# Kernel tuning notes

Measured on AMD Instinct MI355X. Metric: run time of the kernel, lower is better.

The kernel has to match this reference:

```python
import jax, jax.numpy as jnp
import numpy as np

NUM_REGIONS = 29
OUT = 7          # RoIAlign output size
SR = 2           # sampling_ratio
IMG = 1024.0     # input image H = W
LN_EPS = 1e-5


def _layernorm(x, g, b):
    mu = jnp.mean(x, axis=-1, keepdims=True)
    var = jnp.mean(jnp.square(x - mu), axis=-1, keepdims=True)
    return (x - mu) * jax.lax.rsqrt(var + LN_EPS) * g + b


def _roi_align(fm, rois):
    """torchvision roi_align (aligned=False), spatial_scale=1.0, sampling_ratio=SR.
    fm: [B,C,H,W], rois: [B,R,4] (x1,y1,x2,y2 in feature coords). -> [B,R,C,OUT,OUT]"""
    B, C, H, W = fm.shape
    x1, y1, x2, y2 = jnp.moveaxis(rois, -1, 0)            # each [B,R]
    roi_w = jnp.maximum(x2 - x1, 1.0)
    roi_h = jnp.maximum(y2 - y1, 1.0)
    bw = roi_w / OUT
    bh = roi_h / OUT
    # sub-bin offsets: (bin + (s+0.5)/SR) for bin in [0,OUT), s in [0,SR)
    off = jnp.arange(OUT, dtype=jnp.float32)[:, None] + (jnp.arange(SR, dtype=jnp.float32)[None, :] + 0.5) / SR  # [OUT,SR]
    py = y1[..., None, None] + off * bh[..., None, None]  # [B,R,OUT,SR]
    px = x1[..., None, None] + off * bw[..., None, None]  # [B,R,OUT,SR]
    y = py[:, :, :, :, None, None]                        # [B,R,OUT,SR,1,1]
    x = px[:, :, None, None, :, :]                        # [B,R,1,1,OUT,SR]
    valid = (y >= -1.0) & (y <= H) & (x >= -1.0) & (x <= W)
    yc = jnp.clip(y, 0.0, H - 1.0)
    xc = jnp.clip(x, 0.0, W - 1.0)
    y0 = jnp.floor(yc).astype(jnp.int32)
    x0 = jnp.floor(xc).astype(jnp.int32)
    y1i = jnp.minimum(y0 + 1, H - 1)
    x1i = jnp.minimum(x0 + 1, W - 1)
    ly = yc - y0
    lx = xc - x0
    hy = 1.0 - ly
    hx = 1.0 - lx
    gather = jax.vmap(lambda f, yy, xx: f[:, yy, xx])     # per image: [C,H,W] -> [C,...]
    v00 = gather(fm, y0, x0)                              # [B,C,R,OUT,SR,OUT,SR]
    v01 = gather(fm, y0, x1i)
    v10 = gather(fm, y1i, x0)
    v11 = gather(fm, y1i, x1i)
    w00 = (hy * hx)[:, None]
    w01 = (hy * lx)[:, None]
    w10 = (ly * hx)[:, None]
    w11 = (ly * lx)[:, None]
    val = w00 * v00 + w01 * v01 + w10 * v10 + w11 * v11
    val = jnp.where(valid[:, None], val, 0.0)
    pooled = val.mean(axis=(4, 6))                        # average over SRxSR samples -> [B,C,R,OUT,OUT]
    return jnp.transpose(pooled, (0, 2, 1, 3, 4))         # [B,R,C,OUT,OUT]


def setup_inputs() -> dict:
    key = jax.random.key(0)
    ks = jax.random.split(key, 8)
    B, N, C, Hf, Wf, FD = 32, 40, 256, 64, 64, 768
    D = C * OUT * OUT
    feature_maps = jax.random.normal(ks[0], (B, C, Hf, Wf), jnp.float32)
    xy = jax.random.uniform(ks[1], (B, N, 2), jnp.float32) * 900.0
    wh = jax.random.uniform(ks[2], (B, N, 2), jnp.float32) * 100.0 + 16.0
    boxes = jnp.concatenate([xy, xy + wh], axis=-1)       # valid x1,y1,x2,y2 in image coords
    scores = jax.random.uniform(ks[3], (B, N), jnp.float32)
    labels = jax.random.randint(ks[4], (B, N), 0, NUM_REGIONS + 1)
    return {
        'feature_maps': feature_maps,
        'boxes': boxes,
        'scores': scores,
        'labels': labels,
        'w1': jax.random.normal(ks[5], (D, 2048), jnp.float32) * 0.02,
        'b1': jnp.zeros((2048,), jnp.float32),
        'g1': jnp.ones((2048,), jnp.float32),
        'be1': jnp.zeros((2048,), jnp.float32),
        'w2': jax.random.normal(ks[6], (2048, FD), jnp.float32) * 0.02,
        'b2': jnp.zeros((FD,), jnp.float32),
        'g2': jnp.ones((FD,), jnp.float32),
        'be2': jnp.zeros((FD,), jnp.float32),
        'missing_token': jax.random.normal(ks[7], (FD,), jnp.float32),
    }


def reference(feature_maps, boxes, scores, labels, w1, b1, g1, be1, w2, b2, g2, be2, missing_token):
    B, C, Hf, Wf = feature_maps.shape
    R = NUM_REGIONS
    scale = jnp.minimum(Hf / IMG, Wf / IMG)               # scale_factors (same for all images)
    # segmented argmax: best-scoring box per (image, region)
    region_idx = jnp.clip(labels, 1, R) - 1               # [B,N]
    onehot = region_idx[..., None] == jnp.arange(R)       # [B,N,R]
    masked = jnp.where(onehot, scores[..., None], -1.0)   # init best score = -1.0
    detected = jnp.any(onehot, axis=1)                    # [B,R]
    best = jnp.argmax(masked, axis=1)                     # [B,R] first max, matches strict-> loop
    sel = jnp.take_along_axis(boxes, jnp.broadcast_to(best[:, :, None], (B, R, 4)), axis=1)
    rois = sel * scale                                    # [B,R,4] in feature-map coords
    roi_feats = _roi_align(feature_maps, rois)            # [B,R,C,7,7]
    flat = roi_feats.reshape(B * R, C * OUT * OUT)
    h = _layernorm(flat @ w1 + b1, g1, be1)
    h = jax.nn.relu(h)
    h = _layernorm(h @ w2 + b2, g2, be2)                  # [B*R, feature_dim]
    feats = h.reshape(B, R, -1)
    region_features = jnp.where(detected[..., None], feats, missing_token)
    return region_features, detected
```

## Files before the change

### kernel.cpp

```cpp
#include <hip/hip_runtime.h>

typedef __bf16 bf16x8 __attribute__((ext_vector_type(8)));
typedef float f32x4 __attribute__((ext_vector_type(4)));
typedef unsigned short ushort8v __attribute__((ext_vector_type(8)));
typedef unsigned short ushort4v __attribute__((ext_vector_type(4)));

#define BATCH 32
#define NBOX 40
#define CCH 256
#define HF 64
#define WF 64
#define RREG 29
#define OUTP 7
#define MROWS 928
#define DDIM 12544
#define N1DIM 2048
#define FDIM 768
#define PDIM 4096
#define S1 4
#define S2 8

static constexpr size_t OFF_ROIS = 0;
static constexpr size_t OFF_DET  = 16384;
static constexpr size_t OFF_A    = 32768;
static constexpr size_t OFF_W1T  = OFF_A   + (size_t)MROWS * DDIM * 2;
static constexpr size_t OFF_W2T  = OFF_W1T + (size_t)DDIM * N1DIM * 2;
static constexpr size_t OFF_GP   = OFF_W2T + (size_t)N1DIM * FDIM * 2;
static constexpr size_t OFF_FMT  = OFF_GP  + (size_t)S1 * MROWS * N1DIM * 4;
static constexpr size_t OFF_H    = OFF_W1T;

static __device__ __forceinline__ unsigned short f2bf(float f) {
  __bf16 h = (__bf16)f;
  return __builtin_bit_cast(unsigned short, h);
}
static __device__ __forceinline__ float bf2f(unsigned short u) {
  unsigned int x = ((unsigned int)u) << 16;
  return __builtin_bit_cast(float, x);
}
static __device__ __forceinline__ void gload_lds16(const void* g, void* l) {
  __builtin_amdgcn_global_load_lds((const __attribute__((address_space(1))) void*)g,
                                   (__attribute__((address_space(3))) void*)l, 16, 0, 0);
}

__global__ __launch_bounds__(256) void selfmt_kernel(const float* __restrict__ in,
                                                     unsigned short* __restrict__ out,
                                                     const float* __restrict__ boxes,
                                                     const float* __restrict__ scores,
                                                     const int* __restrict__ labels,
                                                     float* __restrict__ rois,
                                                     int* __restrict__ det,
                                                     float* __restrict__ out_det) {
  __shared__ float tile[64][65];
  int bid = blockIdx.x;
  int t = threadIdx.x;
  if (bid >= PDIM / 64 * (CCH / 64) * BATCH) {
    int tid = (bid - PDIM / 64 * (CCH / 64) * BATCH) * 256 + t;
    if (tid >= MROWS) return;
    int b = tid / RREG, r = tid % RREG;
    float bestS = -1.0f;
    int bestN = 0;
    int found = 0;
    for (int n = 0; n < NBOX; ++n) {
      int lab = labels[b * NBOX + n];
      int ri = min(max(lab, 1), RREG) - 1;
      if (ri == r) {
        found = 1;
        float s = scores[b * NBOX + n];
        if (s > bestS) { bestS = s; bestN = n; }
      }
    }
    const float scale = 0.0625f;
    float4 bx = *(const float4*)&boxes[(b * NBOX + bestN) * 4];
    rois[tid * 4 + 0] = bx.x * scale;
    rois[tid * 4 + 1] = bx.y * scale;
    rois[tid * 4 + 2] = bx.z * scale;
    rois[tid * 4 + 3] = bx.w * scale;
    det[tid] = found;
    out_det[tid] = found ? 1.0f : 0.0f;
    return;
  }
  int p0 = (bid & 63) * 64, c0 = ((bid >> 6) & 3) * 64, b = bid >> 8;
  int tx = t & 15, ty = t >> 4;
#pragma unroll
  for (int q = 0; q < 4; ++q) {
    int r = ty + q * 16;
    float4 v = *(const float4*)&in[((long)b * CCH + c0 + r) * PDIM + p0 + tx * 4];
    tile[r][tx * 4 + 0] = v.x;
    tile[r][tx * 4 + 1] = v.y;
    tile[r][tx * 4 + 2] = v.z;
    tile[r][tx * 4 + 3] = v.w;
  }
  __syncthreads();
#pragma unroll
  for (int q = 0; q < 4; ++q) {
    int r = ty + q * 16;
    ushort4v o;
    o[0] = f2bf(tile[tx * 4 + 0][r]);
    o[1] = f2bf(tile[tx * 4 + 1][r]);
    o[2] = f2bf(tile[tx * 4 + 2][r]);
    o[3] = f2bf(tile[tx * 4 + 3][r]);
    *(ushort4v*)&out[((long)b * PDIM + p0 + r) * CCH + c0 + tx * 4] = o;
  }
}

__global__ __launch_bounds__(256) void roiwT_kernel(const unsigned short* __restrict__ fmT,
                                                    const float* __restrict__ rois,
                                                    unsigned short* __restrict__ A,
                                                    const float* __restrict__ w1,
                                                    unsigned short* __restrict__ w1t,
                                                    const float* __restrict__ w2,
                                                    unsigned short* __restrict__ w2t) {
  __shared__ __align__(16) char lds[31360];
  int bid = blockIdx.x;
  int t = threadIdx.x;

  if (bid < MROWS) {
    unsigned short* Arow = (unsigned short*)lds;
    int (*sidx)[4] = (int(*)[4])(lds + 25088);
    float (*swt)[4] = (float(*)[4])(lds + 28224);
    int roi = bid;
    float rx1 = rois[roi * 4 + 0], ry1 = rois[roi * 4 + 1];
    float rx2 = rois[roi * 4 + 2], ry2 = rois[roi * 4 + 3];
    float roiw = fmaxf(rx2 - rx1, 1.f), roih = fmaxf(ry2 - ry1, 1.f);
    float bw = roiw * (1.f / OUTP), bh = roih * (1.f / OUTP);
    if (t < 196) {
      int oy = t / 28, rem = t % 28, ox = rem / 4, s = rem % 4, sy = s >> 1, sx = s & 1;
      float y = ry1 + ((float)oy + ((float)sy + 0.5f) * 0.5f) * bh;
      float x = rx1 + ((float)ox + ((float)sx + 0.5f) * 0.5f) * bw;
      bool valid = (y >= -1.f) && (y <= 64.f) && (x >= -1.f) && (x <= 64.f);
      float yc = fminf(fmaxf(y, 0.f), 63.f);
      float xc = fminf(fmaxf(x, 0.f), 63.f);
      int y0 = (int)floorf(yc), x0 = (int)floorf(xc);
      int y1i = min(y0 + 1, 63), x1i = min(x0 + 1, 63);
      float ly = yc - (float)y0, lx = xc - (float)x0;
      float hy = 1.f - ly, hx = 1.f - lx;
      float m = valid ? 1.f : 0.f;
      swt[t][0] = hy * hx * m;
      swt[t][1] = hy * lx * m;
      swt[t][2] = ly * hx * m;
      swt[t][3] = ly * lx * m;
      sidx[t][0] = (y0 * 64 + x0) * CCH;
      sidx[t][1] = (y0 * 64 + x1i) * CCH;
      sidx[t][2] = (y1i * 64 + x0) * CCH;
      sidx[t][3] = (y1i * 64 + x1i) * CCH;
    }
    __syncthreads();
    int b = roi / RREG;
    int cg = t & 63;
    int sub = t >> 6;
    int start = sub * 12 + min(sub, 1);
    int cnt = sub == 0 ? 13 : 12;
    const unsigned short* base = fmT + (long)b * PDIM * CCH + cg * 4;
    for (int bi = 0; bi < cnt; ++bi) {
      int bin = start + bi;
      float a0 = 0.f, a1 = 0.f, a2 = 0.f, a3 = 0.f;
#pragma unroll
      for (int s = 0; s < 4; ++s) {
        int sid = bin * 4 + s;
#pragma unroll
        for (int tp = 0; tp < 4; ++tp) {
          float w = swt[sid][tp];
          ushort4v v = *(const ushort4v*)(base + sidx[sid][tp]);
          a0 += w * bf2f(v[0]);
          a1 += w * bf2f(v[1]);
          a2 += w * bf2f(v[2]);
          a3 += w * bf2f(v[3]);
        }
      }
      Arow[(cg * 4 + 0) * 49 + bin] = f2bf(a0 * 0.25f);
      Arow[(cg * 4 + 1) * 49 + bin] = f2bf(a1 * 0.25f);
      Arow[(cg * 4 + 2) * 49 + bin] = f2bf(a2 * 0.25f);
      Arow[(cg * 4 + 3) * 49 + bin] = f2bf(a3 * 0.25f);
    }
    __syncthreads();
    const ushort8v* src = (const ushort8v*)Arow;
    ushort8v* dst = (ushort8v*)(A + (long)roi * DDIM);
    for (int i = t; i < DDIM / 8; i += 256) dst[i] = src[i];
    return;
  }

  float (*tile)[65] = (float(*)[65])lds;
  int wb = bid - MROWS;
  const float* in;
  unsigned short* out;
  int K, N, k0, n0;
  if (wb < (DDIM / 64) * (N1DIM / 64)) {
    in = w1; out = w1t; K = DDIM; N = N1DIM;
    k0 = (wb % (DDIM / 64)) * 64;
    n0 = (wb / (DDIM / 64)) * 64;
  } else {
    int r = wb - (DDIM / 64) * (N1DIM / 64);
    in = w2; out = w2t; K = N1DIM; N = FDIM;
    k0 = (r % (N1DIM / 64)) * 64;
    n0 = (r / (N1DIM / 64)) * 64;
  }
  int tx = t & 15, ty = t >> 4;
#pragma unroll
  for (int p = 0; p < 4; ++p) {
    int r = ty + p * 16;
    float4 v = *(const float4*)&in[(long)(k0 + r) * N + n0 + tx * 4];
    tile[r][tx * 4 + 0] = v.x;
    tile[r][tx * 4 + 1] = v.y;
    tile[r][tx * 4 + 2] = v.z;
    tile[r][tx * 4 + 3] = v.w;
  }
  __syncthreads();
#pragma unroll
  for (int p = 0; p < 4; ++p) {
    int r = ty + p * 16;
    ushort4v o;
    o[0] = f2bf(tile[tx * 4 + 0][r]);
    o[1] = f2bf(tile[tx * 4 + 1][r]);
    o[2] = f2bf(tile[tx * 4 + 2][r]);
    o[3] = f2bf(tile[tx * 4 + 3][r]);
    *(ushort4v*)&out[(long)(n0 + r) * K + k0 + tx * 4] = o;
  }
}

__global__ __launch_bounds__(256, 2) void gemm_sk_kernel(const unsigned short* __restrict__ A,
                                                         const unsigned short* __restrict__ Bt,
                                                         float* __restrict__ Cp,
                                                         int M, int N, int K, int kchunk,
                                                         int gy, int q) {
  __shared__ unsigned short As[2 * 128 * 64];
  __shared__ unsigned short Bs[2 * 128 * 64];
  int bid = blockIdx.x;
  int tile = (bid & 7) * q + (bid >> 3);
  int bm = tile & 7;
  int rest = tile >> 3;
  int bn = rest % gy;
  int s = rest / gy;

  int t = threadIdx.x;
  int lane = t & 63, wv = t >> 6;
  int wr = wv >> 1, wc = wv & 1;
  int fr = lane & 15, fq = lane >> 4;

  f32x4 acc[4][4];
#pragma unroll
  for (int m = 0; m < 4; ++m)
#pragma unroll
    for (int n = 0; n < 4; ++n) acc[m][n] = (f32x4){0.f, 0.f, 0.f, 0.f};

  int srow = t >> 3;
  int scol = t & 7;
  int k_begin = s * kchunk;
  int k_end = min(k_begin + kchunk, K);
  int nkt = (k_end - k_begin) >> 6;

  int garow[4], gbrow[4], schunk[4];
#pragma unroll
  for (int i = 0; i < 4; ++i) {
    int row = srow + i * 32;
    schunk[i] = (scol ^ (row & 7)) * 8;
    garow[i] = min(bm * 128 + row, M - 1);
    gbrow[i] = bn * 128 + row;
  }

#define GSTAGE(buf, kt_) do {                                                  \
    int k0_ = k_begin + (kt_) * 64;                                            \
    _Pragma("unroll")                                                          \
    for (int i = 0; i < 4; ++i)                                                \
      gload_lds16(A + (long)garow[i] * K + k0_ + schunk[i],                    \
                  (char*)As + (buf) * 16384 + t * 16 + i * 4096);              \
    _Pragma("unroll")                                                          \
    for (int i = 0; i < 4; ++i)                                                \
      gload_lds16(Bt + (long)gbrow[i] * K + k0_ + schunk[i],                   \
                  (char*)Bs + (buf) * 16384 + t * 16 + i * 4096);              \
  } while (0)

  GSTAGE(0, 0);
  GSTAGE(1, min(1, nkt - 1));

  for (int kt = 0; kt < nkt; ++kt) {
    int cur = kt & 1;
    asm volatile("s_waitcnt vmcnt(8)" ::: "memory");
    __builtin_amdgcn_sched_barrier(0);
    __builtin_amdgcn_s_barrier();
    __builtin_amdgcn_sched_barrier(0);

    const char* Ab = (const char*)As + cur * 16384;
    const char* Bb = (const char*)Bs + cur * 16384;
#pragma unroll
    for (int ks = 0; ks < 2; ++ks) {
      bf16x8 af[4], bfv[4];
#pragma unroll
      for (int m = 0; m < 4; ++m) {
        int row = wr * 64 + m * 16 + fr;
        int bc = (ks * 64 + fq * 16) ^ ((row & 7) << 4);
        af[m] = *(const bf16x8*)(Ab + row * 128 + bc);
      }
#pragma unroll
      for (int n = 0; n < 4; ++n) {
        int row = wc * 64 + n * 16 + fr;
        int bc = (ks * 64 + fq * 16) ^ ((row & 7) << 4);
        bfv[n] = *(const bf16x8*)(Bb + row * 128 + bc);
      }
#pragma unroll
      for (int m = 0; m < 4; ++m)
#pragma unroll
        for (int n = 0; n < 4; ++n)
          acc[m][n] = __builtin_amdgcn_mfma_f32_16x16x32_bf16(af[m], bfv[n], acc[m][n], 0, 0, 0);
    }

    __builtin_amdgcn_sched_barrier(0);
    __builtin_amdgcn_s_barrier();
    __builtin_amdgcn_sched_barrier(0);
    GSTAGE(cur, min(kt + 2, nkt - 1));
  }
#undef GSTAGE

  float* Cb = Cp + (long)s * M * N;
#pragma unroll
  for (int m = 0; m < 4; ++m)
#pragma unroll
    for (int n = 0; n < 4; ++n) {
      int col = bn * 128 + wc * 64 + n * 16 + fr;
#pragma unroll
      for (int j = 0; j < 4; ++j) {
        int row = bm * 128 + wr * 64 + m * 16 + fq * 4 + j;
        if (row < M) Cb[(long)row * N + col] = acc[m][n][j];
      }
    }
}

static __device__ __forceinline__ void block_reduce2(float& a, float& b, float* sm) {
#pragma unroll
  for (int off = 32; off > 0; off >>= 1) {
    a += __shfl_down(a, off);
    b += __shfl_down(b, off);
  }
  int lane = threadIdx.x & 63, wv = threadIdx.x >> 6;
  if (lane == 0) { sm[wv] = a; sm[wv + 4] = b; }
  __syncthreads();
  a = sm[0] + sm[1] + sm[2] + sm[3];
  b = sm[4] + sm[5] + sm[6] + sm[7];
}

__global__ __launch_bounds__(256) void ln1_kernel(const float* __restrict__ X,
                                                  const float* __restrict__ b1,
                                                  const float* __restrict__ g1,
                                                  const float* __restrict__ be1,
                                                  unsigned short* __restrict__ H) {
  __shared__ float sm[8];
  int row = blockIdx.x, t = threadIdx.x;
  float x[8];
  float sum = 0.f, sq = 0.f;
#pragma unroll
  for (int i = 0; i < 8; ++i) {
    int j = t + i * 256;
    float v = b1[j];
#pragma unroll
    for (int s = 0; s < S1; ++s) v += X[((long)s * MROWS + row) * N1DIM + j];
    x[i] = v;
    sum += v;
    sq += v * v;
  }
  block_reduce2(sum, sq, sm);
  float mu = sum * (1.f / N1DIM);
  float inv = rsqrtf(sq * (1.f / N1DIM) - mu * mu + 1e-5f);
#pragma unroll
  for (int i = 0; i < 8; ++i) {
    int j = t + i * 256;
    float y = fmaxf((x[i] - mu) * inv * g1[j] + be1[j], 0.f);
    H[(long)row * N1DIM + j] = f2bf(y);
  }
}

__global__ __launch_bounds__(256) void ln2_kernel(const float* __restrict__ X,
                                                  const float* __restrict__ b2,
                                                  const float* __restrict__ g2,
                                                  const float* __restrict__ be2,
                                                  const float* __restrict__ miss,
                                                  const int* __restrict__ det,
                                                  float* __restrict__ out) {
  __shared__ float sm[8];
  int row = blockIdx.x, t = threadIdx.x;
  float x[3];
  float sum = 0.f, sq = 0.f;
#pragma unroll
  for (int i = 0; i < 3; ++i) {
    int j = t + i * 256;
    float v = b2[j];
#pragma unroll
    for (int s = 0; s < S2; ++s) v += X[((long)s * MROWS + row) * FDIM + j];
    x[i] = v;
    sum += v;
    sq += v * v;
  }
  block_reduce2(sum, sq, sm);
  float mu = sum * (1.f / FDIM);
  float inv = rsqrtf(sq * (1.f / FDIM) - mu * mu + 1e-5f);
  int dv = det[row];
#pragma unroll
  for (int i = 0; i < 3; ++i) {
    int j = t + i * 256;
    float y = (x[i] - mu) * inv * g2[j] + be2[j];
    out[(long)row * FDIM + j] = dv ? y : miss[j];
  }
}

extern "C" void kernel_launch(void* const* d_in, const int* in_sizes, int n_in,
                              void* d_out, int out_size, void* d_ws, size_t ws_size,
                              hipStream_t stream) {
  const float* fm     = (const float*)d_in[0];
  const float* boxes  = (const float*)d_in[1];
  const float* scores = (const float*)d_in[2];
  const int*   labels = (const int*)d_in[3];
  const float* w1     = (const float*)d_in[4];
  const float* b1     = (const float*)d_in[5];
  const float* g1     = (const float*)d_in[6];
  const float* be1    = (const float*)d_in[7];
  const float* w2     = (const float*)d_in[8];
  const float* b2     = (const float*)d_in[9];
  const float* g2     = (const float*)d_in[10];
  const float* be2    = (const float*)d_in[11];
  const float* miss   = (const float*)d_in[12];
  float* out = (float*)d_out;
  char* ws = (char*)d_ws;

  float* rois = (float*)(ws + OFF_ROIS);
  int* det = (int*)(ws + OFF_DET);
  unsigned short* Abf = (unsigned short*)(ws + OFF_A);
  unsigned short* fmT = (unsigned short*)(ws + OFF_FMT);
  unsigned short* w1t = (unsigned short*)(ws + OFF_W1T);
  unsigned short* w2t = (unsigned short*)(ws + OFF_W2T);
  float* Gp = (float*)(ws + OFF_GP);
  unsigned short* Hbf = (unsigned short*)(ws + OFF_H);

  hipLaunchKernelGGL(selfmt_kernel, dim3(8192 + 4), dim3(256), 0, stream,
                     fm, fmT, boxes, scores, labels, rois, det, out + (long)MROWS * FDIM);
  hipLaunchKernelGGL(roiwT_kernel,
                     dim3(MROWS + (DDIM / 64) * (N1DIM / 64) + (N1DIM / 64) * (FDIM / 64)),
                     dim3(256), 0, stream, fmT, rois, Abf, w1, w1t, w2, w2t);
  {
    int nkb = DDIM / 64;
    int kc = ((nkb + S1 - 1) / S1) * 64;
    int gy = N1DIM / 128, nwg = 8 * gy * S1;
    hipLaunchKernelGGL(gemm_sk_kernel, dim3(nwg), dim3(256), 0, stream,
                       Abf, w1t, Gp, MROWS, N1DIM, DDIM, kc, gy, nwg / 8);
  }
  hipLaunchKernelGGL(ln1_kernel, dim3(MROWS), dim3(256), 0, stream, Gp, b1, g1, be1, Hbf);
  {
    int nkb = N1DIM / 64;
    int kc = ((nkb + S2 - 1) / S2) * 64;
    int gy = FDIM / 128, nwg = 8 * gy * S2;
    hipLaunchKernelGGL(gemm_sk_kernel, dim3(nwg), dim3(256), 0, stream,
                       Hbf, w2t, Gp, MROWS, FDIM, N1DIM, kc, gy, nwg / 8);
  }
  hipLaunchKernelGGL(ln2_kernel, dim3(MROWS), dim3(256), 0, stream,
                     Gp, b2, g2, be2, miss, det, out);
}
```

Baseline: 178.0 us.

## Replace first GEMM with 256x256-tile 8-wave split-K kernel

Adds a dedicated GEMM1 kernel using 512-thread workgroups, 256x256 output tiles and a split-K of 7 so that 224 workgroups fill the device. Global-to-LDS loads are interleaved across eight phases, with MFMA blocks raised in priority via setprio. The larger tiles cut redundant A/B reads from global memory and fewer splits reduce partial-sum traffic. In exchange it uses 128 KB of LDS per block (one block per CU) and does a full vmcnt wait every four phases.

```diff
diff --git a/kernel.cpp b/kernel.cpp
--- a/kernel.cpp
+++ b/kernel.cpp
@@ -17,7 +17,7 @@
 #define N1DIM 2048
 #define FDIM 768
 #define PDIM 4096
-#define S1 4
+#define S1 7
 #define S2 8
 
 static constexpr size_t OFF_ROIS = 0;
@@ -217,6 +217,124 @@
   }
 }
 
+__global__ __launch_bounds__(512, 2) void gemm1_8p_kernel(const unsigned short* __restrict__ A,
+                                                          const unsigned short* __restrict__ Bt,
+                                                          float* __restrict__ Cp) {
+  __shared__ __align__(16) char lds[131072];
+  int bid = blockIdx.x;
+  int tile = (bid & 7) * 28 + (bid >> 3);
+  int bm = tile & 3;
+  int bn = (tile >> 2) & 7;
+  int s = tile >> 5;
+  long kb = (long)s * 1792;
+
+  int t = threadIdx.x;
+  int lane = t & 63, wv = t >> 6;
+  int wr = wv >> 2, wc = wv & 3;
+  int fr = lane & 15, fq = lane >> 4;
+  int srow = t >> 3, sch = t & 7;
+
+  f32x4 acc[8][4];
+#pragma unroll
+  for (int m = 0; m < 8; ++m)
+#pragma unroll
+    for (int n = 0; n < 4; ++n) acc[m][n] = (f32x4){0.f, 0.f, 0.f, 0.f};
+
+#define STG(isB, h, ktl, bufs) do {                                            \
+    _Pragma("unroll")                                                          \
+    for (int j = 0; j < 2; ++j) {                                              \
+      int rl = (h) * 128 + srow + j * 64;                                      \
+      long grow = (isB) ? (long)(bn * 256 + rl) : (long)min(bm * 256 + rl, MROWS - 1); \
+      const unsigned short* sp = ((isB) ? Bt : A) + grow * DDIM + kb + (ktl) * 64 \
+                                 + ((sch ^ (rl & 7)) * 8);                     \
+      gload_lds16(sp, lds + ((isB) ? 65536 : 0) + (bufs) * 32768               \
+                          + (h) * 16384 + j * 8192 + t * 16);                  \
+    }                                                                          \
+  } while (0)
+
+  STG(0, 0, 0, 0);
+  STG(0, 1, 0, 0);
+  STG(1, 0, 0, 0);
+  STG(1, 1, 0, 0);
+  asm volatile("s_waitcnt vmcnt(0)" ::: "memory");
+  __builtin_amdgcn_sched_barrier(0);
+  __builtin_amdgcn_s_barrier();
+  __builtin_amdgcn_sched_barrier(0);
+
+  for (int it = 0; it < 14; ++it) {
+#pragma unroll
+    for (int ph = 0; ph < 8; ++ph) {
+      const int half = ph >> 2;
+      const int q = ph & 3, mh = q >> 1, nh = q & 1;
+      const int bufc = half, bufs = half ^ 1;
+
+      bf16x8 af[4][2], bfv[2][2];
+#pragma unroll
+      for (int mi = 0; mi < 4; ++mi) {
+        int row = wr * 128 + (mh * 4 + mi) * 16 + fr;
+#pragma unroll
+        for (int ks = 0; ks < 2; ++ks)
+          af[mi][ks] = *(const bf16x8*)(lds + bufc * 32768 + row * 128
+                                        + ((ks * 64 + fq * 16) ^ ((row & 7) << 4)));
+      }
+#pragma unroll
+      for (int ni = 0; ni < 2; ++ni) {
+        int row = wc * 64 + (nh * 2 + ni) * 16 + fr;
+#pragma unroll
+        for (int ks = 0; ks < 2; ++ks)
+          bfv[ni][ks] = *(const bf16x8*)(lds + 65536 + bufc * 32768 + row * 128
+                                         + ((ks * 64 + fq * 16) ^ ((row & 7) << 4)));
+      }
+
+      {
+        int ktl = min(2 * it + 1 + half, 27);
+        const int op = ph & 3;
+        if (op == 0) STG(0, 0, ktl, bufs);
+        else if (op == 1) STG(0, 1, ktl, bufs);
+        else if (op == 2) STG(1, 0, ktl, bufs);
+        else STG(1, 1, ktl, bufs);
+      }
+
+      if (ph == 3 || ph == 7) {
+        asm volatile("s_waitcnt vmcnt(0)" ::: "memory");
+        __builtin_amdgcn_sched_barrier(0);
+      }
+      __builtin_amdgcn_s_barrier();
+      __builtin_amdgcn_sched_barrier(0);
+      asm volatile("s_waitcnt lgkmcnt(0)" ::: "memory");
+      __builtin_amdgcn_sched_barrier(0);
+
+      __builtin_amdgcn_s_setprio(1);
+#pragma unroll
+      for (int mi = 0; mi < 4; ++mi)
+#pragma unroll
+        for (int ni = 0; ni < 2; ++ni)
+#pragma unroll
+          for (int ks = 0; ks < 2; ++ks)
+            acc[mh * 4 + mi][nh * 2 + ni] = __builtin_amdgcn_mfma_f32_16x16x32_bf16(
+                af[mi][ks], bfv[ni][ks], acc[mh * 4 + mi][nh * 2 + ni], 0, 0, 0);
+      __builtin_amdgcn_s_setprio(0);
+      __builtin_amdgcn_sched_barrier(0);
+      __builtin_amdgcn_s_barrier();
+      __builtin_amdgcn_sched_barrier(0);
+    }
+  }
+#undef STG
+
+  float* Cb = Cp + (long)s * MROWS * N1DIM;
+#pragma unroll
+  for (int m = 0; m < 8; ++m)
+#pragma unroll
+    for (int n = 0; n < 4; ++n) {
+      int col = bn * 256 + wc * 64 + n * 16 + fr;
+#pragma unroll
+      for (int j = 0; j < 4; ++j) {
+        int row = bm * 256 + wr * 128 + m * 16 + fq * 4 + j;
+        if (row < MROWS) Cb[(long)row * N1DIM + col] = acc[m][n][j];
+      }
+    }
+}
+
 __global__ __launch_bounds__(256, 2) void gemm_sk_kernel(const unsigned short* __restrict__ A,
                                                          const unsigned short* __restrict__ Bt,
                                                          float* __restrict__ Cp,
@@ -283,7 +401,7 @@
     const char* Bb = (const char*)Bs + cur * 16384;
 #pragma unroll
     for (int ks = 0; ks < 2; ++ks) {
-      bf16x8 af[4], bfv[4];
+      bf16x8 af[4], bfv2[4];
 #pragma unroll
       for (int m = 0; m < 4; ++m) {
         int row = wr * 64 + m * 16 + fr;
@@ -294,13 +412,13 @@
       for (int n = 0; n < 4; ++n) {
         int row = wc * 64 + n * 16 + fr;
         int bc = (ks * 64 + fq * 16) ^ ((row & 7) << 4);
-        bfv[n] = *(const bf16x8*)(Bb + row * 128 + bc);
+        bfv2[n] = *(const bf16x8*)(Bb + row * 128 + bc);
       }
 #pragma unroll
       for (int m = 0; m < 4; ++m)
 #pragma unroll
         for (int n = 0; n < 4; ++n)
-          acc[m][n] = __builtin_amdgcn_mfma_f32_16x16x32_bf16(af[m], bfv[n], acc[m][n], 0, 0, 0);
+          acc[m][n] = __builtin_amdgcn_mfma_f32_16x16x32_bf16(af[m], bfv2[n], acc[m][n], 0, 0, 0);
     }
 
     __builtin_amdgcn_sched_barrier(0);
@@ -433,13 +551,7 @@
   hipLaunchKernelGGL(roiwT_kernel,
                      dim3(MROWS + (DDIM / 64) * (N1DIM / 64) + (N1DIM / 64) * (FDIM / 64)),
                      dim3(256), 0, stream, fmT, rois, Abf, w1, w1t, w2, w2t);
-  {
-    int nkb = DDIM / 64;
-    int kc = ((nkb + S1 - 1) / S1) * 64;
-    int gy = N1DIM / 128, nwg = 8 * gy * S1;
-    hipLaunchKernelGGL(gemm_sk_kernel, dim3(nwg), dim3(256), 0, stream,
-                       Abf, w1t, Gp, MROWS, N1DIM, DDIM, kc, gy, nwg / 8);
-  }
+  hipLaunchKernelGGL(gemm1_8p_kernel, dim3(224), dim3(512), 0, stream, Abf, w1t, Gp);
   hipLaunchKernelGGL(ln1_kernel, dim3(MROWS), dim3(256), 0, stream, Gp, b1, g1, be1, Hbf);
   {
     int nkb = N1DIM / 64;
```

After: 189.6 us. 6.5% more time.
